# Kernel tuning notes

Hardware: AMD Instinct MI355X
Metric: run time of the kernel (lower is better)

The kernel has to match this reference:

```python
import jax, jax.numpy as jnp
import numpy as np

# -- smoothing / stack constants (mirror __init__ defaults) --
KERNEL_SIZE = 20
SIGMA = 4.0
AMPLITUDE = 0.5
WINDOW = (-10.0, 10.0)
N_POINTS = 350
N_SMOOTH = 331              # 350 - 20 + 1 ('valid' conv)
N_REPEAT = N_POINTS - N_SMOOTH


def setup_inputs() -> dict:
    key = jax.random.key(0)
    k = jax.random.split(key, 6)
    W, A, LA, LB = 2048, 128, 15, 15
    refractive_index = 1.5 + 0.8 * jax.random.uniform(k[0], (N_POINTS,), jnp.float32)
    unknown_layer_thickness = jnp.array([520.0], jnp.float32)        # nm
    thickness_above = 50.0 + 150.0 * jax.random.uniform(k[1], (LA,), jnp.float32)
    thickness_below = 50.0 + 150.0 * jax.random.uniform(k[2], (LB,), jnp.float32)
    fixed_n = 1.3 + 1.2 * jax.random.uniform(k[3], (LA + LB + 2,), jnp.float32)
    fixed_n = fixed_n.at[0].set(1.0)  # incoming medium = air
    wavelengths = jnp.linspace(400.0, 1000.0, W).astype(jnp.float32)  # nm
    angles = jnp.linspace(0.0, 1.0, A).astype(jnp.float32)            # rad
    return dict(refractive_index=refractive_index,
                unknown_layer_thickness=unknown_layer_thickness,
                thickness_above=thickness_above,
                thickness_below=thickness_below,
                fixed_n=fixed_n,
                wavelengths=wavelengths,
                angles=angles)


def _smooth_nk(nk):
    # gaussian smoothing kernel, 'valid' conv: 350 -> 331
    x = jnp.linspace(WINDOW[0], WINDOW[1], KERNEL_SIZE)
    kern = AMPLITUDE * jnp.exp(-(x ** 2) / (2.0 * SIGMA ** 2))
    kern = kern / jnp.sum(kern)
    return jnp.convolve(nk, kern, mode='valid')


def _interface(ri, ti):
    # s-pol interface matrix (1/t) [[1, r], [r, 1]]  -> [..., 2, 2]
    ones = jnp.ones_like(ri)
    I = jnp.stack([jnp.stack([ones, ri], -1), jnp.stack([ri, ones], -1)], -2)
    return I / ti[..., None, None]


def _tmm_s(n_layers, d_interior, wavelengths, angles):
    # n_layers: [L, W] complex; d_interior: [L-2]; returns R, T each [W, A]
    c = n_layers.astype(jnp.complex64)
    nsin = c[0][:, None] * jnp.sin(angles)[None, :]                  # [W, A] Snell invariant
    cos_t = jnp.sqrt(1.0 - (nsin[None] / c[:, :, None]) ** 2)        # [L, W, A]
    q = c[:, :, None] * cos_t                                        # n*cos(theta), [L, W, A]
    denom = q[:-1] + q[1:]
    r = (q[:-1] - q[1:]) / denom                                     # [L-1, W, A]
    t = 2.0 * q[:-1] / denom
    delta = (2.0 * jnp.pi) * q[1:-1] * d_interior[:, None, None] / wavelengths[None, :, None]

    M0 = _interface(r[0], t[0])                                      # [W, A, 2, 2]

    def step(M, inp):
        dlt, ri, ti = inp
        # propagation P = diag(e^{-i d}, e^{+i d}); M@P scales columns of M
        phase = jnp.stack([jnp.exp(-1j * dlt), jnp.exp(1j * dlt)], -1)  # [W, A, 2]
        MP = M * phase[..., None, :]
        M = jnp.einsum('waij,wajk->waik', MP, _interface(ri, ti))
        return M, None

    M, _ = jax.lax.scan(step, M0, (delta, r[1:], t[1:]))
    rr = M[..., 1, 0] / M[..., 0, 0]
    tt = 1.0 / M[..., 0, 0]
    R = jnp.abs(rr) ** 2
    T = jnp.abs(tt) ** 2 * q[-1].real / q[0].real
    return R, T


def reference(refractive_index, unknown_layer_thickness, thickness_above,
              thickness_below, fixed_n, wavelengths, angles):
    LA = thickness_above.shape[0]
    # smooth learnable n, pad tail by repeating last element (repeat_last_element)
    n_smooth = _smooth_nk(refractive_index)                           # [331]
    n_unk = jnp.concatenate([n_smooth, jnp.full((N_REPEAT,), n_smooth[-1])])
    dyn_wl = jnp.linspace(jnp.min(wavelengths), jnp.max(wavelengths), N_SMOOTH)
    dyn_wl = jnp.concatenate([dyn_wl, jnp.full((N_REPEAT,), dyn_wl[-1])])
    # merge_n_data: sample unknown-layer n at the simulation wavelengths
    n_unk_w = jnp.interp(wavelengths, dyn_wl, n_unk)                  # [W]
    W = wavelengths.shape[0]
    fixed_w = jnp.broadcast_to(fixed_n[:, None], (fixed_n.shape[0], W))
    # layer order: incoming, above(LA), unknown, below(LB), outgoing
    n_layers = jnp.concatenate([fixed_w[:LA + 1], n_unk_w[None, :], fixed_w[LA + 1:]], 0)
    d_interior = jnp.concatenate([thickness_above, unknown_layer_thickness, thickness_below])
    R, T = _tmm_s(n_layers, d_interior, wavelengths, angles)
    A_abs = 1.0 - (R + T)  # absorptance per original forward
    # observable = reflectivity
    return R
```

## Files before the change

kernel.cpp:

```cpp
#include <hip/hip_runtime.h>
#include <math.h>

#define NPTS 350
#define NSM  331
#define KS   20
#define LAc  15
#define NLAY 33
#define NIF  32
#define NINT 31
#define NW   2048
#define NA   128
#define WPB  4

__global__ __launch_bounds__(256) void tmm_fused(
    const float* __restrict__ nk,
    const float* __restrict__ d_unk,
    const float* __restrict__ d_above,
    const float* __restrict__ d_below,
    const float* __restrict__ fixed_n,
    const float* __restrict__ wl,
    const float* __restrict__ angles,
    float* __restrict__ out)
{
    __shared__ float2 tab[NIF][NA];
    __shared__ float kern_s[KS];
    __shared__ float ns2_s[NA], qA_s[NA], qB_s[NA];

    const int tid = threadIdx.x;
    const int a = tid & (NA - 1);

    if (tid < NA) {
        const float ang = angles[tid];
        const float nsin = fixed_n[0] * sinf(ang);
        const float ns2 = nsin * nsin;
        ns2_s[tid] = ns2;
        float q[NLAY];
#pragma unroll
        for (int l = 0; l < NLAY; ++l) {
            if (l == LAc + 1) continue;
            const float n = (l <= LAc) ? fixed_n[l] : fixed_n[l - 1];
            q[l] = sqrtf(fmaf(n, n, -ns2));
        }
        qA_s[tid] = q[LAc];
        qB_s[tid] = q[LAc + 2];
#pragma unroll
        for (int j = 0; j < NIF; ++j) {
            float r = 0.0f, qd2 = 0.0f;
            if (j != LAc && j != LAc + 1)
                r = (q[j] - q[j + 1]) * __builtin_amdgcn_rcpf(q[j] + q[j + 1]);
            if (j < NINT && j != LAc) {
                const float dj = (j < LAc) ? d_above[j] : d_below[j - LAc - 1];
                qd2 = 2.0f * q[j + 1] * dj;
            }
            tab[j][tid] = make_float2(r, qd2);
        }
    } else if (tid < NA + KS) {
        const int i = tid - NA;
        const float x = -10.0f + (float)i * (20.0f / 19.0f);
        kern_s[i] = expf(-(x * x) * (1.0f / 32.0f));
    }
    __syncthreads();

    float ksum = 0.0f;
#pragma unroll
    for (int k = 0; k < KS; ++k) ksum += kern_s[k];
    const float kinv = __builtin_amdgcn_rcpf(ksum);

    const int w0 = blockIdx.x * WPB + (tid >> 7);
    const float l0 = wl[0];
    const float scale = (float)(NSM - 1) * __builtin_amdgcn_rcpf(wl[NW - 1] - l0);
    const float ns2 = ns2_s[a];
    const float qA = qA_s[a], qB = qB_s[a];
    const float du = d_unk[0];

    float invlam[2], revu[2], r15[2], r16[2];
    float Nr[2], Ni_[2], Dr[2], Di_[2];
    const float r31 = tab[NIF - 1][a].x;

#pragma unroll
    for (int ci = 0; ci < 2; ++ci) {
        const int w = w0 + 2 * ci;
        const float lam = wl[w];
        float pos = (lam - l0) * scale;
        pos = fminf(fmaxf(pos, 0.0f), (float)(NSM - 1));
        int i0 = (int)pos;
        if (i0 > NSM - 2) i0 = NSM - 2;
        const float f = pos - (float)i0;
        float s0 = 0.0f, s1 = 0.0f;
#pragma unroll
        for (int k = 0; k <= KS; ++k) {
            const float nv = nk[i0 + k];
            if (k < KS) s0 = fmaf(nv, kern_s[k], s0);
            if (k > 0)  s1 = fmaf(nv, kern_s[k - 1], s1);
        }
        const float nunk = fmaf(f, s1 - s0, s0) * kinv;

        const float il = __builtin_amdgcn_rcpf(lam);
        invlam[ci] = il;
        const float qu = sqrtf(fmaf(nunk, nunk, -ns2));
        r15[ci] = (qA - qu) * __builtin_amdgcn_rcpf(qA + qu);
        r16[ci] = (qu - qB) * __builtin_amdgcn_rcpf(qu + qB);
        revu[ci] = 2.0f * qu * du * il;
        Nr[ci] = r31; Ni_[ci] = 0.0f; Dr[ci] = 1.0f; Di_[ci] = 0.0f;
    }

#pragma unroll
    for (int j = NINT - 1; j >= 0; --j) {
        const float2 tj = tab[j][a];
#pragma unroll
        for (int ci = 0; ci < 2; ++ci) {
            const float rev = (j == LAc) ? revu[ci] : tj.y * invlam[ci];
            const float rj = (j == LAc) ? r15[ci]
                           : (j == LAc + 1) ? r16[ci] : tj.x;
            const float fr = __builtin_amdgcn_fractf(rev);
            const float s = __builtin_amdgcn_sinf(fr);
            const float c = __builtin_amdgcn_cosf(fr);
            const float NEr = Nr[ci] * c - Ni_[ci] * s;
            const float NEi = Nr[ci] * s + Ni_[ci] * c;
            Nr[ci] = fmaf(rj, Dr[ci], NEr);
            Ni_[ci] = fmaf(rj, Di_[ci], NEi);
            Dr[ci] = fmaf(rj, NEr, Dr[ci]);
            Di_[ci] = fmaf(rj, NEi, Di_[ci]);
        }
    }

#pragma unroll
    for (int ci = 0; ci < 2; ++ci) {
        const int w = w0 + 2 * ci;
        const float num = fmaf(Nr[ci], Nr[ci], Ni_[ci] * Ni_[ci]);
        const float den = fmaf(Dr[ci], Dr[ci], Di_[ci] * Di_[ci]);
        out[w * NA + a] = num * __builtin_amdgcn_rcpf(den);
    }
}

extern "C" void kernel_launch(void* const* d_in, const int* in_sizes, int n_in,
                              void* d_out, int out_size, void* d_ws, size_t ws_size,
                              hipStream_t stream) {
    const float* nk       = (const float*)d_in[0];
    const float* d_unk    = (const float*)d_in[1];
    const float* d_above  = (const float*)d_in[2];
    const float* d_below  = (const float*)d_in[3];
    const float* fixed_n  = (const float*)d_in[4];
    const float* wl       = (const float*)d_in[5];
    const float* angles   = (const float*)d_in[6];
    float* out = (float*)d_out;

    tmm_fused<<<NW / WPB, 256, 0, stream>>>(nk, d_unk, d_above, d_below,
                                            fixed_n, wl, angles, out);
}
```

Measured before the change: 13.71 us.

## Compute per-angle layer tables in registers, drop shared memory and block barrier

Each thread now computes its own angle's layer admittances, Fresnel coefficients and phase terms, plus the Gaussian kernel, in registers. This replaces the shared-memory table that half the block built before a __syncthreads. It aims to remove the serialized setup phase, the barrier and the LDS traffic. In exchange every thread repeats the per-angle work (33 sqrt, about 30 rcp) that was previously shared by two wavefront groups, and register pressure rises. The launch bounds now request 2 blocks per CU, and sinf is replaced by the hardware sin intrinsic.

After: 12.92 us. 5.8% less time.

```diff
diff --git a/kernel.cpp b/kernel.cpp
--- a/kernel.cpp
+++ b/kernel.cpp
@@ -12,7 +12,7 @@
 #define NA   128
 #define WPB  4
 
-__global__ __launch_bounds__(256) void tmm_fused(
+__global__ __launch_bounds__(256, 2) void tmm_fused(
     const float* __restrict__ nk,
     const float* __restrict__ d_unk,
     const float* __restrict__ d_above,
@@ -22,66 +22,31 @@
     const float* __restrict__ angles,
     float* __restrict__ out)
 {
-    __shared__ float2 tab[NIF][NA];
-    __shared__ float kern_s[KS];
-    __shared__ float ns2_s[NA], qA_s[NA], qB_s[NA];
-
     const int tid = threadIdx.x;
     const int a = tid & (NA - 1);
+    const int w0 = blockIdx.x * WPB + (tid >> 7);
 
-    if (tid < NA) {
-        const float ang = angles[tid];
-        const float nsin = fixed_n[0] * sinf(ang);
-        const float ns2 = nsin * nsin;
-        ns2_s[tid] = ns2;
-        float q[NLAY];
-#pragma unroll
-        for (int l = 0; l < NLAY; ++l) {
-            if (l == LAc + 1) continue;
-            const float n = (l <= LAc) ? fixed_n[l] : fixed_n[l - 1];
-            q[l] = sqrtf(fmaf(n, n, -ns2));
-        }
-        qA_s[tid] = q[LAc];
-        qB_s[tid] = q[LAc + 2];
-#pragma unroll
-        for (int j = 0; j < NIF; ++j) {
-            float r = 0.0f, qd2 = 0.0f;
-            if (j != LAc && j != LAc + 1)
-                r = (q[j] - q[j + 1]) * __builtin_amdgcn_rcpf(q[j] + q[j + 1]);
-            if (j < NINT && j != LAc) {
-                const float dj = (j < LAc) ? d_above[j] : d_below[j - LAc - 1];
-                qd2 = 2.0f * q[j + 1] * dj;
-            }
-            tab[j][tid] = make_float2(r, qd2);
-        }
-    } else if (tid < NA + KS) {
-        const int i = tid - NA;
-        const float x = -10.0f + (float)i * (20.0f / 19.0f);
-        kern_s[i] = expf(-(x * x) * (1.0f / 32.0f));
-    }
-    __syncthreads();
+    const float l0 = wl[0];
+    const float lN = wl[NW - 1];
+    const float lam[2] = { wl[w0], wl[w0 + 2] };
+    const float ang = angles[a];
+    const float du = d_unk[0];
 
+    float kern[KS];
     float ksum = 0.0f;
 #pragma unroll
-    for (int k = 0; k < KS; ++k) ksum += kern_s[k];
+    for (int k = 0; k < KS; ++k) {
+        const float x = -10.0f + (float)k * (20.0f / 19.0f);
+        kern[k] = __expf(-(x * x) * (1.0f / 32.0f));
+        ksum += kern[k];
+    }
     const float kinv = __builtin_amdgcn_rcpf(ksum);
 
-    const int w0 = blockIdx.x * WPB + (tid >> 7);
-    const float l0 = wl[0];
-    const float scale = (float)(NSM - 1) * __builtin_amdgcn_rcpf(wl[NW - 1] - l0);
-    const float ns2 = ns2_s[a];
-    const float qA = qA_s[a], qB = qB_s[a];
-    const float du = d_unk[0];
-
-    float invlam[2], revu[2], r15[2], r16[2];
-    float Nr[2], Ni_[2], Dr[2], Di_[2];
-    const float r31 = tab[NIF - 1][a].x;
-
+    const float scale = (float)(NSM - 1) * __builtin_amdgcn_rcpf(lN - l0);
+    float nunk[2], invlam[2];
 #pragma unroll
     for (int ci = 0; ci < 2; ++ci) {
-        const int w = w0 + 2 * ci;
-        const float lam = wl[w];
-        float pos = (lam - l0) * scale;
+        float pos = (lam[ci] - l0) * scale;
         pos = fminf(fmaxf(pos, 0.0f), (float)(NSM - 1));
         int i0 = (int)pos;
         if (i0 > NSM - 2) i0 = NSM - 2;
@@ -90,36 +55,65 @@
 #pragma unroll
         for (int k = 0; k <= KS; ++k) {
             const float nv = nk[i0 + k];
-            if (k < KS) s0 = fmaf(nv, kern_s[k], s0);
-            if (k > 0)  s1 = fmaf(nv, kern_s[k - 1], s1);
+            if (k < KS) s0 = fmaf(nv, kern[k], s0);
+            if (k > 0)  s1 = fmaf(nv, kern[k - 1], s1);
         }
-        const float nunk = fmaf(f, s1 - s0, s0) * kinv;
+        nunk[ci] = fmaf(f, s1 - s0, s0) * kinv;
+        invlam[ci] = __builtin_amdgcn_rcpf(lam[ci]);
+    }
 
-        const float il = __builtin_amdgcn_rcpf(lam);
-        invlam[ci] = il;
-        const float qu = sqrtf(fmaf(nunk, nunk, -ns2));
-        r15[ci] = (qA - qu) * __builtin_amdgcn_rcpf(qA + qu);
-        r16[ci] = (qu - qB) * __builtin_amdgcn_rcpf(qu + qB);
-        revu[ci] = 2.0f * qu * du * il;
-        Nr[ci] = r31; Ni_[ci] = 0.0f; Dr[ci] = 1.0f; Di_[ci] = 0.0f;
+    const float nsin = fixed_n[0] * __builtin_amdgcn_sinf(ang * 0.15915494309189535f);
+    const float ns2 = nsin * nsin;
+
+    float q[NLAY];
+#pragma unroll
+    for (int l = 0; l < NLAY; ++l) {
+        if (l == LAc + 1) continue;
+        const float n = (l <= LAc) ? fixed_n[l] : fixed_n[l - 1];
+        q[l] = sqrtf(fmaf(n, n, -ns2));
+    }
+
+    float rt[NIF];
+    float qd2[NINT];
+#pragma unroll
+    for (int j = 0; j < NIF; ++j) {
+        if (j == LAc || j == LAc + 1) { rt[j] = 0.0f; continue; }
+        rt[j] = (q[j] - q[j + 1]) * __builtin_amdgcn_rcpf(q[j] + q[j + 1]);
+    }
+#pragma unroll
+    for (int j = 0; j < NINT; ++j) {
+        if (j == LAc) { qd2[j] = 0.0f; continue; }
+        const float dj = (j < LAc) ? d_above[j] : d_below[j - LAc - 1];
+        qd2[j] = 2.0f * q[j + 1] * dj;
+    }
+
+    float r15[2], r16[2], revu[2];
+    float Nr[2], Ni_[2], Dr[2], Di_[2];
+#pragma unroll
+    for (int ci = 0; ci < 2; ++ci) {
+        const float qu = sqrtf(fmaf(nunk[ci], nunk[ci], -ns2));
+        r15[ci] = (q[LAc] - qu) * __builtin_amdgcn_rcpf(q[LAc] + qu);
+        r16[ci] = (qu - q[LAc + 2]) * __builtin_amdgcn_rcpf(qu + q[LAc + 2]);
+        revu[ci] = 2.0f * qu * du * invlam[ci];
+        Nr[ci] = rt[NIF - 1]; Ni_[ci] = 0.0f;
+        Dr[ci] = 1.0f;        Di_[ci] = 0.0f;
     }
 
 #pragma unroll
     for (int j = NINT - 1; j >= 0; --j) {
-        const float2 tj = tab[j][a];
 #pragma unroll
         for (int ci = 0; ci < 2; ++ci) {
-            const float rev = (j == LAc) ? revu[ci] : tj.y * invlam[ci];
+            const float rev = (j == LAc) ? revu[ci] : qd2[j] * invlam[ci];
             const float rj = (j == LAc) ? r15[ci]
-                           : (j == LAc + 1) ? r16[ci] : tj.x;
+                           : (j == LAc + 1) ? r16[ci] : rt[j];
             const float fr = __builtin_amdgcn_fractf(rev);
             const float s = __builtin_amdgcn_sinf(fr);
             const float c = __builtin_amdgcn_cosf(fr);
             const float NEr = Nr[ci] * c - Ni_[ci] * s;
             const float NEi = Nr[ci] * s + Ni_[ci] * c;
-            Nr[ci] = fmaf(rj, Dr[ci], NEr);
+            Nr[ci]  = fmaf(rj, Dr[ci], NEr);
             Ni_[ci] = fmaf(rj, Di_[ci], NEi);
-            Dr[ci] = fmaf(rj, NEr, Dr[ci]);
+            Dr[ci]  = fmaf(rj, NEr, Dr[ci]);
             Di_[ci] = fmaf(rj, NEi, Di_[ci]);
         }
     }
```
